# Kernel tuning notes

Measured on AMD Instinct MI355X. Metric: run time of the kernel, lower is better.

The kernel has to match this reference:

```python
import jax, jax.numpy as jnp
import numpy as np

EPS = 1e-06
LOG_BIAS = 1.0  # config.fire_log_bias


def setup_inputs() -> dict:
    key = jax.random.key(0)
    ks = jax.random.split(key, 5)
    S, H, W = 2048, 12, 32
    x = jax.random.normal(ks[0], (1, S, 768), dtype=jnp.float32)
    w1 = jax.random.normal(ks[1], (W, 1), dtype=jnp.float32) * 0.5
    b1 = jax.random.normal(ks[2], (W,), dtype=jnp.float32) * 0.1
    w2 = jax.random.normal(ks[3], (H, W), dtype=jnp.float32) * 0.2
    b2 = jax.random.normal(ks[4], (H,), dtype=jnp.float32) * 0.1
    c = jnp.float32(0.1)            # fire_init_c, trainable
    L_multiplier = jnp.float32(1.0)  # trainable
    init_L = jnp.float32(512.0)      # non-trainable buffer
    return {"x": x, "w1": w1, "b1": b1, "w2": w2, "b2": b2,
            "c": c, "L_multiplier": L_multiplier, "init_L": init_L}


def reference(x, w1, b1, w2, b2, c, L_multiplier, init_L):
    S = x.shape[1]
    pos = jnp.arange(S, dtype=jnp.float32)
    rel = pos[:, None] - pos[None, :]                      # [S, S]
    abs_rel = jnp.abs(rel) + EPS
    threshold = jnp.abs(L_multiplier * init_L)
    pos_norm = jnp.maximum(pos, threshold)[:, None] + EPS  # [S, 1]
    log_rel = jnp.log(abs_rel * c + LOG_BIAS + EPS)        # [S, S]
    log_norm = jnp.log(jnp.abs(c * pos_norm) + LOG_BIAS + EPS)  # [S, 1]
    nd = log_rel / log_norm                                # [S, S]
    # tiny MLP: Linear(1,W) -> ReLU -> Linear(W,H)
    h = jax.nn.relu(nd[..., None] * w1[:, 0] + b1)         # [S, S, W]
    bias = jnp.einsum('stw,hw->hst', h, w2) + b2[:, None, None]  # [H, S, S]
    return bias[None]                                      # [1, H, S, S]
```

## Files before the change

kernel.cpp:

```cpp
#include <hip/hip_runtime.h>
#include <math.h>


#define SDIM 2048
#define WDIM 32
#define HDIM 12
#define NK 33
#define EPSF 1e-6f
#define LOGB 1.0f

typedef float f32x4 __attribute__((ext_vector_type(4)));

#define WS_T   0
#define WS_AB  64
#define WS_LR  896
#define WS_LN  2944
#define WS_ILN 4992
#define WS_TOTAL 7040

__global__ __launch_bounds__(512) void fire_precompute(
    const float* __restrict__ w1, const float* __restrict__ b1,
    const float* __restrict__ w2, const float* __restrict__ b2,
    const float* __restrict__ cptr, const float* __restrict__ lmptr,
    const float* __restrict__ ilptr, float* __restrict__ ws)
{
    const int tid = threadIdx.x;

    if (blockIdx.x != 0) {
        const int d = ((int)blockIdx.x - 1) * 512 + tid;
        const float c = cptr[0];
        ws[WS_LR + d] = logf(fmaf((float)d + EPSF, c, LOGB + EPSF));
        const float thr = fabsf(lmptr[0] * ilptr[0]);
        const float pn  = fmaxf((float)d, thr) + EPSF;
        const float ln  = logf(fabsf(c * pn) + LOGB + EPSF);
        ws[WS_LN  + d] = ln;
        ws[WS_ILN + d] = 1.0f / ln;
        return;
    }

    __shared__ float traw[WDIM], w1s[WDIM], b1s[WDIM];
    __shared__ int rnk[WDIM], neg[WDIM];

    if (tid < WDIM) {
        float a = w1[tid], b = b1[tid];
        w1s[tid] = a; b1s[tid] = b;
        float t; int isneg;
        if (a > 0.f)      { t = -b / a; isneg = 0; }
        else if (a < 0.f) { t = -b / a; isneg = 1; }
        else {
            t = (b > 0.f) ? -INFINITY : INFINITY; isneg = 0;
        }
        traw[tid] = t; neg[tid] = isneg;
    }
    __syncthreads();

    if (tid < WDIM) {
        float t = traw[tid];
        int r = 0;
        for (int v = 0; v < WDIM; ++v) {
            float tv = traw[v];
            if (tv < t || (tv == t && v < tid)) r++;
        }
        rnk[tid] = r;
        ws[WS_T + r] = t;
    } else if (tid < 64) {
        ws[WS_T + tid] = INFINITY;
    }
    __syncthreads();

    if (tid < NK * HDIM) {
        const int k = tid % NK;
        const int h = tid / NK;
        float a = 0.f, bb = 0.f;
        for (int w = 0; w < WDIM; ++w) {
            const bool active = neg[w] ? (rnk[w] >= k) : (rnk[w] < k);
            if (active) {
                float w2v = w2[h * WDIM + w];
                a  += w2v * w1s[w];
                bb += w2v * b1s[w];
            }
        }
        bb += b2[h];
        ws[WS_AB + (k * HDIM + h) * 2 + 0] = a;
        ws[WS_AB + (k * HDIM + h) * 2 + 1] = bb;
    }
}

__global__ __launch_bounds__(512) void fire_main(
    const float* __restrict__ ws, float* __restrict__ out)
{
    __shared__ float sTp[64];
    __shared__ float sAB[2 * NK * HDIM];
    __shared__ __align__(16) float sLR[SDIM];
    const int tid = threadIdx.x;
    const int i = blockIdx.x;

    const float ln_i = ws[WS_LN  + i];
    const float ivl  = ws[WS_ILN + i];

    ((f32x4*)sLR)[tid] = ((const f32x4*)(ws + WS_LR))[tid];
    if (tid < 64) sTp[tid] = ws[WS_T + tid] * ln_i;
    for (int idx = tid; idx < 2 * NK * HDIM; idx += 512) {
        float v = ws[WS_AB + idx];
        if ((idx & 1) == 0) v *= ivl;
        sAB[idx] = v;
    }
    __syncthreads();

    const int j0 = tid * 4;
    float lrv[4];
    int kk[4];
    #pragma unroll
    for (int e = 0; e < 4; ++e) {
        int j = j0 + e;
        int dd = i - j; if (dd < 0) dd = -dd;
        float x = sLR[dd];
        int k = 0;
        if (x > sTp[k + 31]) k += 32;
        if (x > sTp[k + 15]) k += 16;
        if (x > sTp[k + 7])  k += 8;
        if (x > sTp[k + 3])  k += 4;
        if (x > sTp[k + 1])  k += 2;
        if (x > sTp[k])      k += 1;
        kk[e] = k;
        lrv[e] = x;
    }

    const size_t base = (size_t)i * SDIM + (size_t)j0;
    #pragma unroll
    for (int h = 0; h < HDIM; ++h) {
        f32x4 v;
        #pragma unroll
        for (int e = 0; e < 4; ++e) {
            int idx = (kk[e] * HDIM + h) * 2;
            v[e] = fmaf(sAB[idx], lrv[e], sAB[idx + 1]);
        }
        __builtin_nontemporal_store(v, (f32x4*)(out + (size_t)h * SDIM * SDIM + base));
    }
}

extern "C" void kernel_launch(void* const* d_in, const int* in_sizes, int n_in,
                              void* d_out, int out_size, void* d_ws, size_t ws_size,
                              hipStream_t stream)
{
    const float* w1 = (const float*)d_in[1];
    const float* b1 = (const float*)d_in[2];
    const float* w2 = (const float*)d_in[3];
    const float* b2 = (const float*)d_in[4];
    const float* c  = (const float*)d_in[5];
    const float* lm = (const float*)d_in[6];
    const float* il = (const float*)d_in[7];
    float* ws  = (float*)d_ws;
    float* out = (float*)d_out;

    fire_precompute<<<5, 512, 0, stream>>>(w1, b1, w2, b2, c, lm, il, ws);
    fire_main<<<SDIM, 512, 0, stream>>>(ws, out);
}
```

Before: 225.6 us.

## Fuse precompute into main kernel and vectorize per-segment coefficient loads

```diff
diff --git a/kernel.cpp b/kernel.cpp
--- a/kernel.cpp
+++ b/kernel.cpp
@@ -11,38 +11,39 @@
 
 typedef float f32x4 __attribute__((ext_vector_type(4)));
 
-#define WS_T   0
-#define WS_AB  64
-#define WS_LR  896
-#define WS_LN  2944
-#define WS_ILN 4992
-#define WS_TOTAL 7040
-
-__global__ __launch_bounds__(512) void fire_precompute(
+__global__ __launch_bounds__(512) void fire_fused(
     const float* __restrict__ w1, const float* __restrict__ b1,
     const float* __restrict__ w2, const float* __restrict__ b2,
     const float* __restrict__ cptr, const float* __restrict__ lmptr,
-    const float* __restrict__ ilptr, float* __restrict__ ws)
+    const float* __restrict__ ilptr, float* __restrict__ out)
 {
+    __shared__ __align__(16) float sLR[SDIM];
+    __shared__ __align__(16) float sAB[NK * 24];
+    __shared__ float sTp[64];
+    __shared__ float traw[WDIM], w1s[WDIM], b1s[WDIM];
+    __shared__ int   rnk[WDIM], neg[WDIM];
+    __shared__ float sLn[2];
+
     const int tid = threadIdx.x;
+    const int i   = blockIdx.x;
+    const float c = cptr[0];
 
-    if (blockIdx.x != 0) {
-        const int d = ((int)blockIdx.x - 1) * 512 + tid;
-        const float c = cptr[0];
-        ws[WS_LR + d] = logf(fmaf((float)d + EPSF, c, LOGB + EPSF));
+    {
+        const int d0 = tid * 4;
+        #pragma unroll
+        for (int e = 0; e < 4; ++e) {
+            const float d = (float)(d0 + e);
+            sLR[d0 + e] = logf(fmaf(d + EPSF, c, LOGB + EPSF));
+        }
+    }
+    if (tid == 0) {
         const float thr = fabsf(lmptr[0] * ilptr[0]);
-        const float pn  = fmaxf((float)d, thr) + EPSF;
+        const float pn  = fmaxf((float)i, thr) + EPSF;
         const float ln  = logf(fabsf(c * pn) + LOGB + EPSF);
-        ws[WS_LN  + d] = ln;
-        ws[WS_ILN + d] = 1.0f / ln;
-        return;
+        sLn[0] = ln; sLn[1] = 1.0f / ln;
     }
-
-    __shared__ float traw[WDIM], w1s[WDIM], b1s[WDIM];
-    __shared__ int rnk[WDIM], neg[WDIM];
-
     if (tid < WDIM) {
-        float a = w1[tid], b = b1[tid];
+        const float a = w1[tid], b = b1[tid];
         w1s[tid] = a; b1s[tid] = b;
         float t; int isneg;
         if (a > 0.f)      { t = -b / a; isneg = 0; }
@@ -55,66 +56,45 @@
     __syncthreads();
 
     if (tid < WDIM) {
-        float t = traw[tid];
+        const float t = traw[tid];
         int r = 0;
         for (int v = 0; v < WDIM; ++v) {
-            float tv = traw[v];
+            const float tv = traw[v];
             if (tv < t || (tv == t && v < tid)) r++;
         }
         rnk[tid] = r;
-        ws[WS_T + r] = t;
+        sTp[r] = t * sLn[0];
     } else if (tid < 64) {
-        ws[WS_T + tid] = INFINITY;
+        sTp[tid] = INFINITY;
     }
     __syncthreads();
 
     if (tid < NK * HDIM) {
-        const int k = tid % NK;
-        const int h = tid / NK;
+        const int k = tid / HDIM;
+        const int h = tid % HDIM;
         float a = 0.f, bb = 0.f;
         for (int w = 0; w < WDIM; ++w) {
             const bool active = neg[w] ? (rnk[w] >= k) : (rnk[w] < k);
             if (active) {
-                float w2v = w2[h * WDIM + w];
+                const float w2v = w2[h * WDIM + w];
                 a  += w2v * w1s[w];
                 bb += w2v * b1s[w];
             }
         }
         bb += b2[h];
-        ws[WS_AB + (k * HDIM + h) * 2 + 0] = a;
-        ws[WS_AB + (k * HDIM + h) * 2 + 1] = bb;
-    }
-}
-
-__global__ __launch_bounds__(512) void fire_main(
-    const float* __restrict__ ws, float* __restrict__ out)
-{
-    __shared__ float sTp[64];
-    __shared__ float sAB[2 * NK * HDIM];
-    __shared__ __align__(16) float sLR[SDIM];
-    const int tid = threadIdx.x;
-    const int i = blockIdx.x;
-
-    const float ln_i = ws[WS_LN  + i];
-    const float ivl  = ws[WS_ILN + i];
-
-    ((f32x4*)sLR)[tid] = ((const f32x4*)(ws + WS_LR))[tid];
-    if (tid < 64) sTp[tid] = ws[WS_T + tid] * ln_i;
-    for (int idx = tid; idx < 2 * NK * HDIM; idx += 512) {
-        float v = ws[WS_AB + idx];
-        if ((idx & 1) == 0) v *= ivl;
-        sAB[idx] = v;
+        sAB[k * 24 + h * 2 + 0] = a * sLn[1];
+        sAB[k * 24 + h * 2 + 1] = bb;
     }
     __syncthreads();
 
     const int j0 = tid * 4;
     float lrv[4];
-    int kk[4];
+    int   kk[4];
     #pragma unroll
     for (int e = 0; e < 4; ++e) {
-        int j = j0 + e;
+        const int j = j0 + e;
         int dd = i - j; if (dd < 0) dd = -dd;
-        float x = sLR[dd];
+        const float x = sLR[dd];
         int k = 0;
         if (x > sTp[k + 31]) k += 32;
         if (x > sTp[k + 15]) k += 16;
@@ -128,14 +108,16 @@
 
     const size_t base = (size_t)i * SDIM + (size_t)j0;
     #pragma unroll
-    for (int h = 0; h < HDIM; ++h) {
-        f32x4 v;
+    for (int hp = 0; hp < 6; ++hp) {
+        f32x4 va, vb;
         #pragma unroll
         for (int e = 0; e < 4; ++e) {
-            int idx = (kk[e] * HDIM + h) * 2;
-            v[e] = fmaf(sAB[idx], lrv[e], sAB[idx + 1]);
+            const f32x4 ab = *(const f32x4*)&sAB[kk[e] * 24 + hp * 4];
+            va[e] = fmaf(ab.x, lrv[e], ab.y);
+            vb[e] = fmaf(ab.z, lrv[e], ab.w);
         }
-        __builtin_nontemporal_store(v, (f32x4*)(out + (size_t)h * SDIM * SDIM + base));
+        *(f32x4*)(out + (size_t)(2 * hp)     * SDIM * SDIM + base) = va;
+        *(f32x4*)(out + (size_t)(2 * hp + 1) * SDIM * SDIM + base) = vb;
     }
 }
 
@@ -150,9 +132,7 @@
     const float* c  = (const float*)d_in[5];
     const float* lm = (const float*)d_in[6];
     const float* il = (const float*)d_in[7];
-    float* ws  = (float*)d_ws;
     float* out = (float*)d_out;
 
-    fire_precompute<<<5, 512, 0, stream>>>(w1, b1, w2, b2, c, lm, il, ws);
-    fire_main<<<SDIM, 512, 0, stream>>>(ws, out);
+    fire_fused<<<SDIM, 512, 0, stream>>>(w1, b1, w2, b2, c, lm, il, out);
 }
```

Result: no change. 226.2 us (+0.3%).
